# Kernel optimization log

Measured on AMD Instinct MI355X. Metric: run time of the kernel, lower is better.

The kernel has to match this reference:

```python
import jax, jax.numpy as jnp
import numpy as np

B, S, D, H = 2, 2048, 1024, 16
HD = D // H
EPS = 1e-8
LN_EPS = 1e-5


def setup_inputs() -> dict:
    key = jax.random.key(0)
    ks = jax.random.split(key, 12)
    std = 0.02
    inp = {}
    inp["x"] = jax.random.normal(ks[0], (B, S, D), jnp.float32)
    # q/k/v/out projections (stored (in, out); y = x @ W + b)
    inp["Wq"] = jax.random.normal(ks[1], (D, D), jnp.float32) * std
    inp["bq"] = jnp.zeros((D,), jnp.float32)
    inp["Wk"] = jax.random.normal(ks[2], (D, D), jnp.float32) * std
    inp["bk"] = jnp.zeros((D,), jnp.float32)
    inp["Wv"] = jax.random.normal(ks[3], (D, D), jnp.float32) * std
    inp["bv"] = jnp.zeros((D,), jnp.float32)
    inp["Wo"] = jax.random.normal(ks[4], (D, D), jnp.float32) * std
    inp["bo"] = jnp.zeros((D,), jnp.float32)
    # 4 DeltaResidualBlocks stacked on axis 0: [q, k, v, out]
    inp["dWk"] = jax.random.normal(ks[5], (4, D, D), jnp.float32) * 0.01  # k_proj, no bias
    inp["dbw"] = jnp.zeros((4, D), jnp.float32)                           # beta_proj weight (init zeros)
    inp["dbb"] = jnp.full((4,), -4.0, jnp.float32)                        # beta_proj bias
    inp["dWv"] = jax.random.normal(ks[6], (4, D), jnp.float32) * 0.02     # v_proj weight (d_v=1)
    inp["dbv"] = jnp.zeros((4,), jnp.float32)                             # v_proj bias
    inp["ln_g"] = jnp.ones((D,), jnp.float32)
    inp["ln_b"] = jnp.zeros((D,), jnp.float32)
    return inp


def reference(x, Wq, bq, Wk, bk, Wv, bv, Wo, bo, dWk, dbw, dbb, dWv, dbv, ln_g, ln_b):
    def delta(h, v_in, i):
        # DeltaResidualBlock (d_v=1): h + beta * k * (v - k.h)
        k_raw = jnp.einsum('bsd,de->bse', h, dWk[i])
        k = k_raw / (jnp.linalg.norm(k_raw, axis=-1, keepdims=True) + EPS)
        beta = 2.0 * jax.nn.sigmoid(jnp.einsum('bsd,d->bs', h, dbw[i])[..., None] + dbb[i])  # (B,S,1)
        v = jnp.einsum('bsd,d->bs', v_in, dWv[i])[..., None] + dbv[i]                        # (B,S,1)
        k_dot_h = jnp.sum(k * h, axis=-1, keepdims=True)
        return h + beta * k * (v - k_dot_h)

    q = delta(x, x @ Wq + bq, 0)
    k = delta(x, x @ Wk + bk, 1)
    v = delta(x, x @ Wv + bv, 2)

    # (B,S,D) -> (B,H,S,HD)
    q = q.reshape(B, S, H, HD).transpose(0, 2, 1, 3)
    k = k.reshape(B, S, H, HD).transpose(0, 2, 1, 3)
    v = v.reshape(B, S, H, HD).transpose(0, 2, 1, 3)

    scale = HD ** -0.5
    scores = jnp.einsum('bhqd,bhkd->bhqk', q, k) * scale
    attn = jax.nn.softmax(scores, axis=-1)
    out = jnp.einsum('bhqk,bhkd->bhqd', attn, v)
    out = out.transpose(0, 2, 1, 3).reshape(B, S, D)
    out = out @ Wo + bo

    y = delta(x, out, 3)

    # LayerNorm
    mu = jnp.mean(y, axis=-1, keepdims=True)
    var = jnp.mean((y - mu) ** 2, axis=-1, keepdims=True)
    y = (y - mu) / jnp.sqrt(var + LN_EPS) * ln_g + ln_b
    return y
```

## Files before the change

### kernel.cpp

```cpp
#include <hip/hip_runtime.h>

#define BB 2
#define SS 2048
#define DD 1024
#define HH 16
#define HD 64
#define MM (BB*SS)
#define KC 4
#define KT_PER (SS/64/KC)
#define KSTEPS (DD/64)

typedef unsigned short u16;
typedef __attribute__((ext_vector_type(8))) short bf16x8;
typedef __attribute__((ext_vector_type(4))) float f32x4;

typedef __attribute__((address_space(1))) const unsigned int* gas_t;
typedef __attribute__((address_space(3))) unsigned int* las_t;

#ifndef __has_builtin
#define __has_builtin(x) 0
#endif
#if __has_builtin(__builtin_amdgcn_exp2f)
#define EXP2F(x) __builtin_amdgcn_exp2f(x)
#else
#define EXP2F(x) __expf((x)*0.6931471805599453f)
#endif
#define QSCALE 0.18033688011112042f

__device__ __forceinline__ void gl_lds16(const u16* g, u16* l){
  __builtin_amdgcn_global_load_lds((gas_t)g, (las_t)l, 16, 0, 0);
}

__device__ __forceinline__ u16 f2bf(float f){
  unsigned u = __float_as_uint(f);
  u += 0x7FFF + ((u >> 16) & 1);
  return (u16)(u >> 16);
}
__device__ __forceinline__ float bf2f(u16 h){
  return __uint_as_float(((unsigned)h) << 16);
}
__device__ __forceinline__ float dot4f(float4 a, float4 b){
  return a.x*b.x + a.y*b.y + a.z*b.z + a.w*b.w;
}

#define SBAR() do { \
  __builtin_amdgcn_sched_barrier(0); \
  __builtin_amdgcn_s_barrier(); \
  __builtin_amdgcn_sched_barrier(0); \
} while (0)

#define NB_CONV 2048
#define NB_TRAN 2048
#define NB_PREC 4100
#define NB_PREP (NB_CONV+NB_TRAN+NB_PREC)
__global__ void prep_kernel(const float* __restrict__ x, u16* __restrict__ xb,
                            const float* __restrict__ dWk, u16* __restrict__ dWkT,
                            const float* __restrict__ Wq_, const float* __restrict__ bq_,
                            const float* __restrict__ Wk_, const float* __restrict__ bk_,
                            const float* __restrict__ Wv_, const float* __restrict__ bv_,
                            const float* __restrict__ Wo_, const float* __restrict__ bo_,
                            const float* __restrict__ dWv, const float* __restrict__ dbv,
                            float* __restrict__ wv, float* __restrict__ cv) {
  int blk = blockIdx.x, t = threadIdx.x;
  if (blk < NB_CONV) {
    size_t idx = ((size_t)blk*256 + t)*8;
    float4 a = *(const float4*)(x + idx);
    float4 b = *(const float4*)(x + idx + 4);
    union { u16 u[8]; uint4 v; } pk;
    pk.u[0]=f2bf(a.x); pk.u[1]=f2bf(a.y); pk.u[2]=f2bf(a.z); pk.u[3]=f2bf(a.w);
    pk.u[4]=f2bf(b.x); pk.u[5]=f2bf(b.y); pk.u[6]=f2bf(b.z); pk.u[7]=f2bf(b.w);
    *(uint4*)(xb + idx) = pk.v;
    return;
  }
  blk -= NB_CONV;
  if (blk < NB_TRAN) {
    int xi = blk & 3, rest = blk >> 2;
    int ck = rest & 127, i = rest >> 7;
    int n  = xi*256 + t;
    const float* src = dWk + (size_t)i*DD*DD + (size_t)ck*8*DD + n;
    union { u16 u[8]; uint4 v; } pk;
    #pragma unroll
    for (int e=0;e<8;e++) pk.u[e] = f2bf(src[(size_t)e*DD]);
    *(uint4*)(dWkT + (size_t)i*DD*DD + (size_t)n*DD + ck*8) = pk.v;
    return;
  }
  blk -= NB_TRAN;
  {
    int i = blk / 1025, row = blk % 1025;
    const float* W    = (i==0)?Wq_:(i==1)?Wk_:(i==2)?Wv_:Wo_;
    const float* bvec = (i==0)?bq_:(i==1)?bk_:(i==2)?bv_:bo_;
    const float* s = dWv + i*DD;
    __shared__ float red[256];
    float acc = 0.f;
    if (row < DD) {
      const float* r = W + (size_t)row * DD;
      for (int e = t; e < DD; e += 256) acc += r[e]*s[e];
    } else {
      for (int e = t; e < DD; e += 256) acc += bvec[e]*s[e];
    }
    red[t] = acc; __syncthreads();
    for (int off=128; off>0; off>>=1){ if(t<off) red[t]+=red[t+off]; __syncthreads(); }
    if (t==0) {
      if (row < DD) wv[i*DD + row] = red[0];
      else          cv[i] = red[0] + dbv[i];
    }
  }
}

__device__ __forceinline__ void stage_half(const u16* __restrict__ g, u16* l,
                                           int k0, int half, int isA,
                                           int wid, int lane) {
  const int lr = lane>>3, lc = lane&7;
  #pragma unroll
  for (int j=0; j<2; j++) {
    const int u = wid*2 + j;
    int grow;
    if (isA) grow = ((u & 8) ? 128 + ((u & 7)<<3) : (u<<3)) + (half<<6);
    else     grow = ((u>>2)<<6) + ((u&3)<<3) + (half<<5);
    gl_lds16(g + (size_t)(grow + lr)*DD + k0 + ((lc^lr)<<3), l + grow*64);
  }
}

__device__ __forceinline__ void lda4(const u16* base, int row0, int q15, int quad,
                                     int sw, bf16x8 (&f)[4][2]) {
  #pragma unroll
  for (int mf=0; mf<4; mf++)
    #pragma unroll
    for (int kk=0; kk<2; kk++)
      f[mf][kk] = *(const bf16x8*)(base + (row0 + mf*16 + q15)*64 + (((kk*4+quad)^sw)<<3));
}
__device__ __forceinline__ void ldb2(const u16* base, int row0, int q15, int quad,
                                     int sw, bf16x8 (&f)[2][2]) {
  #pragma unroll
  for (int nf=0; nf<2; nf++)
    #pragma unroll
    for (int kk=0; kk<2; kk++)
      f[nf][kk] = *(const bf16x8*)(base + (row0 + nf*16 + q15)*64 + (((kk*4+quad)^sw)<<3));
}
__device__ __forceinline__ void quad_mfma(const bf16x8 (&af)[4][2], const bf16x8 (&bfr)[2][2],
                                          f32x4 (&acc)[8][4], int mo, int no) {
  __builtin_amdgcn_s_setprio(1);
  #pragma unroll
  for (int kk=0; kk<2; kk++)
    #pragma unroll
    for (int mf=0; mf<4; mf++)
      #pragma unroll
      for (int nf=0; nf<2; nf++)
        acc[mo+mf][no+nf] = __builtin_amdgcn_mfma_f32_16x16x32_bf16(
            af[mf][kk], bfr[nf][kk], acc[mo+mf][no+nf], 0,0,0);
  __builtin_amdgcn_s_setprio(0);
}

__global__ __launch_bounds__(512, 2) void gemm_dwk_8ph(const u16* __restrict__ xb,
                          const u16* __restrict__ Bt, u16* __restrict__ kraw) {
  const int bid = blockIdx.x;
  const int xcd = bid & 7, rr = bid >> 3;
  const int i = xcd >> 1;
  const int mt = ((xcd & 1) << 3) | (rr & 7);
  const int ntile = rr >> 3;
  const int m0 = mt << 8, n0 = ntile << 8;
  const u16* Ab = xb + (size_t)m0*DD;
  const u16* Bb = Bt + (size_t)i*DD*DD + (size_t)n0*DD;
  u16* C = kraw + (size_t)i*MM*DD;

  const int t = threadIdx.x, wid = t>>6, lane = t&63;
  const int q15 = lane&15, quad = lane>>4, sw = q15&7;
  const int wm = wid>>2, wn = wid&3;
  const int arow = wm<<7, brow = wn<<6;

  __shared__ u16 As[2][256*64];
  __shared__ u16 Bs[2][256*64];

  f32x4 acc[8][4];
  #pragma unroll
  for (int a=0;a<8;a++)
    #pragma unroll
    for (int b2=0;b2<4;b2++) acc[a][b2] = (f32x4){0.f,0.f,0.f,0.f};

  stage_half(Ab, As[0], 0,  0, 1, wid, lane);
  stage_half(Bb, Bs[0], 0,  0, 0, wid, lane);
  stage_half(Bb, Bs[0], 0,  1, 0, wid, lane);
  stage_half(Ab, As[0], 0,  1, 1, wid, lane);
  stage_half(Ab, As[1], 64, 0, 1, wid, lane);
  stage_half(Bb, Bs[1], 64, 0, 0, wid, lane);
  stage_half(Bb, Bs[1], 64, 1, 0, wid, lane);
  __builtin_amdgcn_sched_barrier(0);
  asm volatile("s_waitcnt vmcnt(6)" ::: "memory");
  SBAR();

  for (int u=0; u<KSTEPS; ++u) {
    const int cur = u & 1;
    const u16* Ac = As[cur]; const u16* Bc = Bs[cur];
    const int k1 = (u+1 < KSTEPS ? u+1 : KSTEPS-1) << 6;
    const int k2 = (u+2 < KSTEPS ? u+2 : KSTEPS-1) << 6;
    bf16x8 a0[4][2], a1[4][2], b0[2][2], b1[2][2];

    lda4(Ac, arow,      q15, quad, sw, a0);
    ldb2(Bc, brow,      q15, quad, sw, b0);
    stage_half(Ab, As[cur^1], k1, 1, 1, wid, lane);
    SBAR();
    quad_mfma(a0, b0, acc, 0, 0);
    SBAR();
    ldb2(Bc, brow+32,   q15, quad, sw, b1);
    stage_half(Ab, As[cur], k2, 0, 1, wid, lane);
    SBAR();
    quad_mfma(a0, b1, acc, 0, 2);
    SBAR();
    lda4(Ac, arow+64,   q15, quad, sw, a1);
    stage_half(Bb, Bs[cur], k2, 0, 0, wid, lane);
    SBAR();
    quad_mfma(a1, b1, acc, 4, 2);
    SBAR();
    stage_half(Bb, Bs[cur], k2, 1, 0, wid, lane);
    __builtin_amdgcn_sched_barrier(0);
    asm volatile("s_waitcnt vmcnt(6)" ::: "memory");
    SBAR();
    quad_mfma(a1, b0, acc, 4, 0);
    SBAR();
  }

  #pragma unroll
  for (int mf=0; mf<8; mf++)
    #pragma unroll
    for (int nf=0; nf<4; nf++)
      #pragma unroll
      for (int r4=0; r4<4; r4++) {
        int m = m0 + arow + mf*16 + quad*4 + r4;
        int n = n0 + brow + nf*16 + q15;
        C[(size_t)m*DD + n] = f2bf(acc[mf][nf][r4]);
      }
}

__global__ void delta_qkv_kernel(const float* __restrict__ x, const u16* __restrict__ kraw,
                                 const float* __restrict__ dbw, const float* __restrict__ dbb,
                                 const float* __restrict__ wv, const float* __restrict__ cv,
                                 u16* __restrict__ qk, float* __restrict__ Vw) {
  int m = blockIdx.x, t = threadIdx.x, w = t>>6, lane = t&63;
  const float* xr = x + (size_t)m*DD;
  float4 xv = *(const float4*)(xr + t*4);
  __shared__ float4 part[3][4];
  float4 kvs[3];
  #pragma unroll
  for (int i=0;i<3;i++) {
    ushort4 ku = *(const ushort4*)(kraw + (size_t)i*MM*DD + (size_t)m*DD + t*4);
    float4 kv = make_float4(bf2f(ku.x), bf2f(ku.y), bf2f(ku.z), bf2f(ku.w));
    kvs[i] = kv;
    float4 bwv = *(const float4*)(dbw + i*DD + t*4);
    float4 wvv = *(const float4*)(wv  + i*DD + t*4);
    float4 red = make_float4(dot4f(kv,kv), dot4f(kv,xv), dot4f(xv,bwv), dot4f(xv,wvv));
    #pragma unroll
    for (int off=32; off>0; off>>=1) {
      red.x += __shfl_xor(red.x, off);
      red.y += __shfl_xor(red.y, off);
      red.z += __shfl_xor(red.z, off);
      red.w += __shfl_xor(red.w, off);
    }
    if (lane==0) part[i][w] = red;
  }
  __syncthreads();
  float cc[3];
  #pragma unroll
  for (int i=0;i<3;i++) {
    float4 r0=part[i][0], r1=part[i][1], r2=part[i][2], r3=part[i][3];
    float s0=r0.x+r1.x+r2.x+r3.x, s1=r0.y+r1.y+r2.y+r3.y;
    float s2=r0.z+r1.z+r2.z+r3.z, s3=r0.w+r1.w+r2.w+r3.w;
    float nrmE = sqrtf(s0) + 1e-8f;
    float kdh  = s1 / nrmE;
    float beta = 2.f / (1.f + __expf(-(s2 + dbb[i])));
    float vs   = s3 + cv[i];
    cc[i] = beta * (vs - kdh) / nrmE;
  }
  {
    float c = cc[0]; float4 kv = kvs[0];
    ushort4 ou;
    ou.x = f2bf((xv.x + c*kv.x)*QSCALE); ou.y = f2bf((xv.y + c*kv.y)*QSCALE);
    ou.z = f2bf((xv.z + c*kv.z)*QSCALE); ou.w = f2bf((xv.w + c*kv.w)*QSCALE);
    *(ushort4*)(qk + (size_t)m*DD + t*4) = ou;
  }
  {
    float c = cc[1]; float4 kv = kvs[1];
    ushort4 ou;
    ou.x = f2bf(xv.x + c*kv.x); ou.y = f2bf(xv.y + c*kv.y);
    ou.z = f2bf(xv.z + c*kv.z); ou.w = f2bf(xv.w + c*kv.w);
    *(ushort4*)(qk + (size_t)MM*DD + (size_t)m*DD + t*4) = ou;
  }
  {
    float c = cc[2]; float4 kv = kvs[2];
    float4 vv = make_float4(xv.x + c*kv.x, xv.y + c*kv.y, xv.z + c*kv.z, xv.w + c*kv.w);
    float4 w3 = *(const float4*)(wv + 3*DD + t*4);
    float s = dot4f(vv, w3);
    #pragma unroll
    for (int off=1; off<16; off<<=1) s += __shfl_xor(s, off);
    if ((lane & 15) == 0) {
      int head = t >> 4;
      int b = m >> 11, srow = m & (SS-1);
      Vw[((size_t)(b*HH + head))*SS + srow] = s;
    }
  }
}

__global__ __launch_bounds__(256, 6) void flash_mfma(const u16* __restrict__ qb,
     const u16* __restrict__ kb, const float* __restrict__ Vw,
     float* __restrict__ l_arr, float* __restrict__ pv_arr) {
  const int qt = blockIdx.x, h = blockIdx.y;
  const int b = blockIdx.z >> 2, kc = blockIdx.z & 3;
  const int t = threadIdx.x, w = t>>6, lane = t&63, q15 = lane&15, quad = lane>>4;
  const int lr = lane>>3, lc = lane&7, gsw = lc ^ lr;
  const int sw = q15 & 7;
  __shared__ u16 Ks[3][64*64];
  __shared__ float Vws[KT_PER*64];
  const size_t hb = (size_t)h*HD;
  const u16* kbase = kb + (size_t)(b*SS + kc*KT_PER*64)*DD + hb;
  const float* vwb = Vw + (size_t)(b*HH + h)*SS + kc*KT_PER*64;

  bf16x8 qf[2];
  {
    const u16* qrow = qb + (size_t)(b*SS + qt*64 + w*16 + q15)*DD + hb;
    qf[0] = *(const bf16x8*)(qrow + quad*8);
    qf[1] = *(const bf16x8*)(qrow + 32 + quad*8);
  }
  if (t < KT_PER*64/4) {
    float4 v = *(const float4*)(vwb + t*4);
    *(float4*)(&Vws[t*4]) = v;
  }
  #pragma unroll
  for (int j=0; j<2; j++) {
    int r = (w*2+j)*8 + lr;
    gl_lds16(kbase + (size_t)r*DD + gsw*8, &Ks[0][((w*2+j)*8)*64]);
    gl_lds16(kbase + (size_t)(64 + r)*DD + gsw*8, &Ks[1][((w*2+j)*8)*64]);
  }
  float l_acc = 0.f, pv_acc = 0.f;
  __syncthreads();

  #pragma unroll
  for (int kt=0; kt<KT_PER; kt++) {
    if (kt+2 < KT_PER) {
      #pragma unroll
      for (int j=0; j<2; j++) {
        int r = (w*2+j)*8 + lr;
        gl_lds16(kbase + (size_t)((kt+2)*64 + r)*DD + gsw*8,
                 &Ks[(kt+2)%3][((w*2+j)*8)*64]);
      }
    }
    f32x4 Sacc[4];
    #pragma unroll
    for (int rt=0; rt<4; rt++) Sacc[rt] = (f32x4){0.f,0.f,0.f,0.f};
    #pragma unroll
    for (int kk=0; kk<2; kk++) {
      #pragma unroll
      for (int rt=0; rt<4; rt++) {
        bf16x8 kf = *(bf16x8*)(&Ks[kt%3][(rt*16+q15)*64 + ((kk*4+quad)^sw)*8]);
        Sacc[rt] = __builtin_amdgcn_mfma_f32_16x16x32_bf16(kf, qf[kk], Sacc[rt], 0,0,0);
      }
    }
    #pragma unroll
    for (int rt=0; rt<4; rt++) {
      float4 va = *(const float4*)(&Vws[kt*64 + rt*16 + quad*4]);
      float p0 = EXP2F(fminf(Sacc[rt][0], 30.f));
      float p1 = EXP2F(fminf(Sacc[rt][1], 30.f));
      float p2 = EXP2F(fminf(Sacc[rt][2], 30.f));
      float p3 = EXP2F(fminf(Sacc[rt][3], 30.f));
      l_acc  += (p0 + p1) + (p2 + p3);
      pv_acc += p0*va.x + p1*va.y + p2*va.z + p3*va.w;
    }
    if (kt < KT_PER-1) {
      __builtin_amdgcn_sched_barrier(0);
      if (kt+2 < KT_PER) asm volatile("s_waitcnt vmcnt(2)" ::: "memory");
      else               asm volatile("s_waitcnt vmcnt(0)" ::: "memory");
      __builtin_amdgcn_s_barrier();
      __builtin_amdgcn_sched_barrier(0);
    }
  }
  l_acc  += __shfl_xor(l_acc, 16);  l_acc  += __shfl_xor(l_acc, 32);
  pv_acc += __shfl_xor(pv_acc, 16); pv_acc += __shfl_xor(pv_acc, 32);
  if (quad == 0) {
    int tok = b*SS + qt*64 + w*16 + q15;
    size_t idx = ((size_t)kc*MM + tok)*HH + h;
    l_arr[idx]  = l_acc;
    pv_arr[idx] = pv_acc;
  }
}

__global__ void final_kernel(const float* __restrict__ x, const u16* __restrict__ kraw3,
                             const float* __restrict__ l_arr, const float* __restrict__ pv_arr,
                             const float* __restrict__ dbw, const float* __restrict__ dbb,
                             const float* __restrict__ cv,
                             const float* __restrict__ ln_g, const float* __restrict__ ln_b,
                             float* __restrict__ out) {
  int m = blockIdx.x, t = threadIdx.x, w = t>>6, lane = t&63;
  const float* xr = x     + (size_t)m*DD;
  const u16*   kr = kraw3 + (size_t)m*DD;
  float4 xv  = *(const float4*)(xr + t*4);
  ushort4 ku = *(const ushort4*)(kr + t*4);
  float4 kv  = make_float4(bf2f(ku.x), bf2f(ku.y), bf2f(ku.z), bf2f(ku.w));
  float4 bwv = *(const float4*)(dbw + 3*DD + t*4);
  __shared__ float4 part[4];
  __shared__ float2 part2[4];
  __shared__ float v3s;
  if (t < 16) {
    float lsum = 0.f, psum = 0.f;
    #pragma unroll
    for (int kc=0; kc<KC; kc++) {
      size_t idx = ((size_t)kc*MM + m)*HH + t;
      lsum += l_arr[idx];
      psum += pv_arr[idx];
    }
    float val = psum / lsum;
    #pragma unroll
    for (int off=1; off<16; off<<=1) val += __shfl_xor(val, off);
    if (t==0) v3s = val;
  }
  float4 red = make_float4(dot4f(kv,kv), dot4f(kv,xv), dot4f(xv,bwv), 0.f);
  #pragma unroll
  for (int off=32; off>0; off>>=1) {
    red.x += __shfl_xor(red.x, off);
    red.y += __shfl_xor(red.y, off);
    red.z += __shfl_xor(red.z, off);
  }
  if (lane==0) part[w] = red;
  __syncthreads();
  float4 r0=part[0], r1=part[1], r2=part[2], r3=part[3];
  float s0=r0.x+r1.x+r2.x+r3.x, s1=r0.y+r1.y+r2.y+r3.y, s2=r0.z+r1.z+r2.z+r3.z;
  float nrmE = sqrtf(s0) + 1e-8f;
  float kdh  = s1 / nrmE;
  float beta = 2.f / (1.f + __expf(-(s2 + dbb[3])));
  float v3   = v3s + cv[3];
  float c = beta * (v3 - kdh) / nrmE;
  float y0 = xv.x + c*kv.x, y1 = xv.y + c*kv.y, y2 = xv.z + c*kv.z, y3 = xv.w + c*kv.w;
  float2 rr = make_float2(y0+y1+y2+y3, y0*y0+y1*y1+y2*y2+y3*y3);
  #pragma unroll
  for (int off=32; off>0; off>>=1) {
    rr.x += __shfl_xor(rr.x, off);
    rr.y += __shfl_xor(rr.y, off);
  }
  if (lane==0) part2[w] = rr;
  __syncthreads();
  float ssum = part2[0].x+part2[1].x+part2[2].x+part2[3].x;
  float ssq  = part2[0].y+part2[1].y+part2[2].y+part2[3].y;
  float mu   = ssum * (1.f/DD);
  float var  = ssq * (1.f/DD) - mu*mu;
  float rstd = rsqrtf(var + 1e-5f);
  float4 g  = *(const float4*)(ln_g + t*4);
  float4 bb = *(const float4*)(ln_b + t*4);
  float4 ov;
  ov.x = (y0-mu)*rstd*g.x + bb.x;
  ov.y = (y1-mu)*rstd*g.y + bb.y;
  ov.z = (y2-mu)*rstd*g.z + bb.z;
  ov.w = (y3-mu)*rstd*g.w + bb.w;
  *(float4*)(out + (size_t)m*DD + t*4) = ov;
}

extern "C" void kernel_launch(void* const* d_in, const int* in_sizes, int n_in,
                              void* d_out, int out_size, void* d_ws, size_t ws_size,
                              hipStream_t stream) {
  const float* x    = (const float*)d_in[0];
  const float* Wq_  = (const float*)d_in[1];
  const float* bq_  = (const float*)d_in[2];
  const float* Wk_  = (const float*)d_in[3];
  const float* bk_  = (const float*)d_in[4];
  const float* Wv_  = (const float*)d_in[5];
  const float* bv_  = (const float*)d_in[6];
  const float* Wo_  = (const float*)d_in[7];
  const float* bo_  = (const float*)d_in[8];
  const float* dWk  = (const float*)d_in[9];
  const float* dbw  = (const float*)d_in[10];
  const float* dbb  = (const float*)d_in[11];
  const float* dWv  = (const float*)d_in[12];
  const float* dbv  = (const float*)d_in[13];
  const float* ln_g = (const float*)d_in[14];
  const float* ln_b = (const float*)d_in[15];
  float* out = (float*)d_out;
  char* WS = (char*)d_ws;

  float* wv     = (float*)WS;
  float* cv     = (float*)(WS + 16384);
  u16*   kraw   = (u16*)  (WS + 16640);
  u16*   qk     = (u16*)  (WS + 16640 + (size_t)4*MM*DD*2);
  u16*   dWkT   = (u16*)  (WS + 16640 + (size_t)6*MM*DD*2);
  u16*   xb     = (u16*)  (WS + 16640 + (size_t)6*MM*DD*2 + (size_t)4*DD*DD*2);
  char*  tail   = WS + 16640 + (size_t)6*MM*DD*2 + (size_t)8*DD*DD*2;
  float* Vw     = (float*)tail;
  float* l_arr  = (float*)(tail + (size_t)BB*HH*SS*4);
  float* pv_arr = (float*)(tail + (size_t)BB*HH*SS*4 + (size_t)KC*MM*HH*4);

  prep_kernel<<<NB_PREP, 256, 0, stream>>>(
      x, xb, dWk, dWkT, Wq_,bq_,Wk_,bk_,Wv_,bv_,Wo_,bo_, dWv, dbv, wv, cv);
  gemm_dwk_8ph<<<256, 512, 0, stream>>>(xb, dWkT, kraw);
  delta_qkv_kernel<<<MM, 256, 0, stream>>>(x, kraw, dbw, dbb, wv, cv, qk, Vw);
  flash_mfma<<<dim3(SS/64, HH, BB*KC), 256, 0, stream>>>(
      qk, qk + (size_t)MM*DD, Vw, l_arr, pv_arr);
  final_kernel<<<MM, 256, 0, stream>>>(x, kraw + 3*(size_t)MM*DD, l_arr, pv_arr,
                                       dbw, dbb, cv, ln_g, ln_b, out);
}
```

Baseline: 225.9 us.

## Cut barriers in dWk GEMM main loop and vectorize bf16 epilogue stores

Restructures the dWk GEMM main loop from eight workgroup barriers per k-step to two, grouping LDS fragment reads and global-to-LDS staging into fewer phases with pairs of MFMA batches between them. It swaps the MFMA operand order so each lane holds four consecutive output columns, which lets the epilogue write packed 8-byte bf16 stores instead of scalar 16-bit stores. This removes synchronization overhead and uncoalesced writes. In exchange it raises register pressure from holding more fragments at once, and the reordered LDS reuse depends on the vmcnt and barrier placement still being correct.

```diff
diff --git a/kernel.cpp b/kernel.cpp
--- a/kernel.cpp
+++ b/kernel.cpp
@@ -43,6 +43,7 @@
   return a.x*b.x + a.y*b.y + a.z*b.z + a.w*b.w;
 }
 
+#define SB0() __builtin_amdgcn_sched_barrier(0)
 #define SBAR() do { \
   __builtin_amdgcn_sched_barrier(0); \
   __builtin_amdgcn_s_barrier(); \
@@ -147,7 +148,7 @@
       #pragma unroll
       for (int nf=0; nf<2; nf++)
         acc[mo+mf][no+nf] = __builtin_amdgcn_mfma_f32_16x16x32_bf16(
-            af[mf][kk], bfr[nf][kk], acc[mo+mf][no+nf], 0,0,0);
+            bfr[nf][kk], af[mf][kk], acc[mo+mf][no+nf], 0,0,0);
   __builtin_amdgcn_s_setprio(0);
 }
 
@@ -184,7 +185,7 @@
   stage_half(Ab, As[1], 64, 0, 1, wid, lane);
   stage_half(Bb, Bs[1], 64, 0, 0, wid, lane);
   stage_half(Bb, Bs[1], 64, 1, 0, wid, lane);
-  __builtin_amdgcn_sched_barrier(0);
+  SB0();
   asm volatile("s_waitcnt vmcnt(6)" ::: "memory");
   SBAR();
 
@@ -195,40 +196,41 @@
     const int k2 = (u+2 < KSTEPS ? u+2 : KSTEPS-1) << 6;
     bf16x8 a0[4][2], a1[4][2], b0[2][2], b1[2][2];
 
-    lda4(Ac, arow,      q15, quad, sw, a0);
-    ldb2(Bc, brow,      q15, quad, sw, b0);
+    lda4(Ac, arow,    q15, quad, sw, a0);
+    ldb2(Bc, brow,    q15, quad, sw, b0);
+    ldb2(Bc, brow+32, q15, quad, sw, b1);
     stage_half(Ab, As[cur^1], k1, 1, 1, wid, lane);
-    SBAR();
+    SB0();
     quad_mfma(a0, b0, acc, 0, 0);
-    SBAR();
-    ldb2(Bc, brow+32,   q15, quad, sw, b1);
+    quad_mfma(a0, b1, acc, 0, 2);
+    SB0();
+    lda4(Ac, arow+64, q15, quad, sw, a1);
+    SB0();
+    __builtin_amdgcn_s_barrier();
+    SB0();
     stage_half(Ab, As[cur], k2, 0, 1, wid, lane);
-    SBAR();
-    quad_mfma(a0, b1, acc, 0, 2);
-    SBAR();
-    lda4(Ac, arow+64,   q15, quad, sw, a1);
     stage_half(Bb, Bs[cur], k2, 0, 0, wid, lane);
-    SBAR();
+    stage_half(Bb, Bs[cur], k2, 1, 0, wid, lane);
+    SB0();
     quad_mfma(a1, b1, acc, 4, 2);
-    SBAR();
-    stage_half(Bb, Bs[cur], k2, 1, 0, wid, lane);
-    __builtin_amdgcn_sched_barrier(0);
+    quad_mfma(a1, b0, acc, 4, 0);
+    SB0();
     asm volatile("s_waitcnt vmcnt(6)" ::: "memory");
-    SBAR();
-    quad_mfma(a1, b0, acc, 4, 0);
-    SBAR();
-  }
-
-  #pragma unroll
-  for (int mf=0; mf<8; mf++)
-    #pragma unroll
-    for (int nf=0; nf<4; nf++)
-      #pragma unroll
-      for (int r4=0; r4<4; r4++) {
-        int m = m0 + arow + mf*16 + quad*4 + r4;
-        int n = n0 + brow + nf*16 + q15;
-        C[(size_t)m*DD + n] = f2bf(acc[mf][nf][r4]);
-      }
+    __builtin_amdgcn_s_barrier();
+    SB0();
+  }
+
+  #pragma unroll
+  for (int mf=0; mf<8; mf++) {
+    const int m = m0 + arow + mf*16 + q15;
+    u16* Crow = C + (size_t)m*DD + n0 + brow;
+    #pragma unroll
+    for (int nf=0; nf<4; nf++) {
+      unsigned u0 = (unsigned)f2bf(acc[mf][nf][0]) | ((unsigned)f2bf(acc[mf][nf][1]) << 16);
+      unsigned u1 = (unsigned)f2bf(acc[mf][nf][2]) | ((unsigned)f2bf(acc[mf][nf][3]) << 16);
+      *(uint2*)(Crow + nf*16 + quad*4) = make_uint2(u0, u1);
+    }
+  }
 }
 
 __global__ void delta_qkv_kernel(const float* __restrict__ x, const u16* __restrict__ kraw,
```

After: 226.9 us. Within noise of the previous version (+0.5%).
